# Kernel optimization log

Measured on AMD Instinct MI355X. Metric: run time of the kernel, lower is better.

Reference implementation:

```python
import jax, jax.numpy as jnp
import numpy as np

HIDDEN_DIM = 1024
NUM_HEADS = 16
HEAD_DIM = HIDDEN_DIM // NUM_HEADS
SCALAR_NORM = float(np.sqrt(HIDDEN_DIM / NUM_HEADS))


def setup_inputs() -> dict:
    key = jax.random.key(0)
    k1, k2 = jax.random.split(key)
    B, N, D = 2, 2048, HIDDEN_DIM
    x = jax.random.normal(k1, (B, N, D), dtype=jnp.float32)
    # torch Linear weight shape: (3D, D); xavier_uniform-like scale
    limit = float(np.sqrt(6.0 / (D + 3 * D)))
    W_qkv = jax.random.uniform(k2, (3 * D, D), dtype=jnp.float32, minval=-limit, maxval=limit)
    return {"x": x, "W_qkv": W_qkv}


def reference(x, W_qkv):
    b, n, d = x.shape
    h, hd = NUM_HEADS, HEAD_DIM
    qkv = x @ W_qkv.T  # (B, N, 3D)
    q, k, v = jnp.split(qkv, 3, axis=-1)
    # (B, H, N, hd)
    q = q.reshape(b, n, h, hd).transpose(0, 2, 1, 3)
    k = k.reshape(b, n, h, hd).transpose(0, 2, 1, 3)
    v = v.reshape(b, n, h, hd).transpose(0, 2, 1, 3)
    scores = jnp.einsum('bhik,bhjk->bhij', q, k) / SCALAR_NORM
    attn = jax.nn.softmax(scores, axis=-1)
    out = jnp.einsum('bhij,bhjk->bhik', attn, v)
    return out.transpose(0, 2, 1, 3).reshape(b, n, d)
```

## Files before the change

kernel.cpp:

```cpp
#include <hip/hip_runtime.h>
#include <hip/hip_bf16.h>

#define SEQ 2048
#define DMODEL 1024
#define NHEADS 16
#define HD 64
#define BATCH 2

typedef short bf16x8 __attribute__((ext_vector_type(8)));
typedef float f32x4 __attribute__((ext_vector_type(4)));

static __device__ inline ushort f2bf(float f) {
    unsigned u = __float_as_uint(f);
    return (ushort)((u + 0x7fffu + ((u >> 16) & 1u)) >> 16);
}

static __device__ inline unsigned pk2bf(float a, float b) {
    __hip_bfloat162 h = __float22bfloat162_rn(make_float2(a, b));
    union { __hip_bfloat162 h; unsigned u; } c; c.h = h;
    return c.u;
}

static __device__ inline void async16(const ushort* g, ushort* l) {
    __builtin_amdgcn_global_load_lds((const __attribute__((address_space(1))) void*)g,
                                     (__attribute__((address_space(3))) void*)l, 16, 0, 0);
}

__global__ void cvt2(const float* __restrict__ a, ushort* __restrict__ da, int na,
                     const float* __restrict__ b, ushort* __restrict__ db, int nb) {
    long i = (long)(blockIdx.x * blockDim.x + threadIdx.x) * 4;
    const float* s; ushort* d;
    if (i < na) { s = a + i; d = da + i; }
    else { long j = i - na; if (j >= nb) return; s = b + j; d = db + j; }
    float4 v = *(const float4*)s;
    ushort4 o; o.x = f2bf(v.x); o.y = f2bf(v.y); o.z = f2bf(v.z); o.w = f2bf(v.w);
    *(ushort4*)d = o;
}

union GemmSmem {
    struct { ushort A[128 * 64]; ushort B[128 * 64]; } st;
    ushort C[128 * 128];
};

__global__ __launch_bounds__(256) void qkv_gemm(
        const ushort* __restrict__ X, const ushort* __restrict__ W,
        ushort* __restrict__ Qd, ushort* __restrict__ Kd, ushort* __restrict__ Vd) {
    __shared__ GemmSmem sm;
    const int t = threadIdx.x;
    const int lane = t & 63, l15 = lane & 15, quad = lane >> 4;
    const int w = t >> 6, wm = w >> 1, wn = w & 1;
    const int gm = blockIdx.x, gn = blockIdx.y;
    const int srow = t >> 3, scol = (t & 7) * 8;

    f32x4 acc[4][4] = {};

    for (int kt = 0; kt < 16; ++kt) {
        const int k0 = kt * 64;
        __syncthreads();
#pragma unroll
        for (int inst = 0; inst < 4; ++inst) {
            async16(&X[(gm * 128 + inst * 32 + srow) * 1024 + k0 + scol], &sm.st.A[inst * 2048 + t * 8]);
            async16(&W[(gn * 128 + inst * 32 + srow) * 1024 + k0 + scol], &sm.st.B[inst * 2048 + t * 8]);
        }
        __syncthreads();
#pragma unroll
        for (int ks = 0; ks < 2; ++ks) {
            const int kk = ks * 32 + quad * 8;
            bf16x8 af[4], bfr[4];
#pragma unroll
            for (int i = 0; i < 4; ++i) {
                af[i]  = *(const bf16x8*)&sm.st.A[(wm * 64 + i * 16 + l15) * 64 + kk];
                bfr[i] = *(const bf16x8*)&sm.st.B[(wn * 64 + i * 16 + l15) * 64 + kk];
            }
#pragma unroll
            for (int i = 0; i < 4; ++i)
#pragma unroll
                for (int j = 0; j < 4; ++j)
                    acc[i][j] = __builtin_amdgcn_mfma_f32_16x16x32_bf16(af[i], bfr[j], acc[i][j], 0, 0, 0);
        }
    }

    __syncthreads();
    const float sc = (gn < 8) ? (0.125f * 1.44269504f) : 1.0f;
#pragma unroll
    for (int i = 0; i < 4; ++i)
#pragma unroll
        for (int reg = 0; reg < 4; ++reg) {
            const int row = wm * 64 + i * 16 + quad * 4 + reg;
            const int sw = (row & 7) * 8;
#pragma unroll
            for (int jp = 0; jp < 4; jp += 2) {
                unsigned u = pk2bf(acc[i][jp][reg] * sc, acc[i][jp + 1][reg] * sc);
                sm.C[row * 128 + ((wn * 64 + jp * 16 + l15) ^ sw)] = (ushort)u;
                sm.C[row * 128 + ((wn * 64 + (jp + 1) * 16 + l15) ^ sw)] = (ushort)(u >> 16);
            }
        }
    __syncthreads();

    const int which = gn >> 3;
    ushort* dst = (which == 0) ? Qd : ((which == 1) ? Kd : Vd);
    const int rloc = t >> 4, l = t & 15;
#pragma unroll
    for (int pass = 0; pass < 8; ++pass) {
        const int r = pass * 16 + rloc;
        bf16x8 v = *(const bf16x8*)&sm.C[r * 128 + ((l * 8) ^ ((r & 7) * 8))];
        const int ng = gm * 128 + r;
        const int b = ng >> 11, n = ng & 2047;
        const int cl = (gn * 128 + l * 8) & 1023;
        const int h = cl >> 6, hd = cl & 63;
        *(bf16x8*)&dst[(((b * NHEADS + h) * SEQ) + n) * HD + hd] = v;
    }
}

__global__ __launch_bounds__(256) void tr_v(const ushort* __restrict__ src, ushort* __restrict__ dst) {
    __shared__ ushort sT[64][72];
    const int t = threadIdx.x;
    const int bh = blockIdx.y, nt = blockIdx.x;
    const int r0 = t >> 3, c8 = (t & 7) * 8;
    const ushort* sp = src + ((long)bh * SEQ + nt * 64) * HD;
#pragma unroll
    for (int rr = 0; rr < 64; rr += 32)
        *(bf16x8*)&sT[rr + r0][c8] = *(const bf16x8*)&sp[(rr + r0) * HD + c8];
    __syncthreads();
    ushort* dp = dst + (long)bh * HD * SEQ + nt * 64;
#pragma unroll
    for (int rr = 0; rr < 64; rr += 32) {
        const int hd = rr + r0;
        bf16x8 v;
#pragma unroll
        for (int j = 0; j < 8; ++j) v[j] = (short)sT[c8 + j][hd];
        *(bf16x8*)&dp[(long)hd * SEQ + c8] = v;
    }
}

__global__ __launch_bounds__(128, 2) void attn_kernel(
        const ushort* __restrict__ Q, const ushort* __restrict__ K,
        const ushort* __restrict__ VT, float* __restrict__ O) {
    __shared__ ushort sK[64][72];
    __shared__ ushort sVT[64][72];
    __shared__ ushort sP[64][72];
    const int t = threadIdx.x;
    const int lane = t & 63, l15 = lane & 15, quad = lane >> 4;
    const int w = t >> 6;
    const int qt = blockIdx.x, bh = blockIdx.y;
    const ushort* Qp = Q + ((long)bh * SEQ + qt * 64) * HD;
    const ushort* Kp = K + (long)bh * SEQ * HD;
    const ushort* Vp = VT + (long)bh * HD * SEQ;
    const int r0 = t >> 3, c8 = (t & 7) * 8;

    bf16x8 aq[2][2];
#pragma unroll
    for (int st = 0; st < 2; ++st)
#pragma unroll
        for (int kc = 0; kc < 2; ++kc)
            aq[st][kc] = *(const bf16x8*)&Qp[(w * 32 + st * 16 + l15) * HD + kc * 32 + quad * 8];

    f32x4 accO[2][4] = {};
    f32x4 accL[2] = {};
    bf16x8 ones;
#pragma unroll
    for (int j = 0; j < 8; ++j) ones[j] = (short)0x3F80;

    for (int kt = 0; kt < 32; ++kt) {
        __syncthreads();
#pragma unroll
        for (int rr = 0; rr < 64; rr += 16) {
            *(bf16x8*)&sK[rr + r0][c8]  = *(const bf16x8*)&Kp[(kt * 64 + rr + r0) * HD + c8];
            *(bf16x8*)&sVT[rr + r0][c8] = *(const bf16x8*)&Vp[(rr + r0) * SEQ + kt * 64 + c8];
        }
        __syncthreads();

        f32x4 s[2][4];
#pragma unroll
        for (int st = 0; st < 2; ++st)
#pragma unroll
            for (int nb = 0; nb < 4; ++nb) {
                f32x4 z = {};
                z = __builtin_amdgcn_mfma_f32_16x16x32_bf16(aq[st][0], *(const bf16x8*)&sK[nb * 16 + l15][quad * 8], z, 0, 0, 0);
                z = __builtin_amdgcn_mfma_f32_16x16x32_bf16(aq[st][1], *(const bf16x8*)&sK[nb * 16 + l15][32 + quad * 8], z, 0, 0, 0);
                s[st][nb] = z;
            }

#pragma unroll
        for (int st = 0; st < 2; ++st)
#pragma unroll
            for (int r = 0; r < 4; ++r) {
                const int row = w * 32 + st * 16 + quad * 4 + r;
#pragma unroll
                for (int nb = 0; nb < 4; nb += 2) {
                    unsigned u = pk2bf(exp2f(s[st][nb][r]), exp2f(s[st][nb + 1][r]));
                    sP[row][(nb * 16 + l15) ^ (quad << 4)] = (ushort)u;
                    sP[row][((nb + 1) * 16 + l15) ^ (quad << 4)] = (ushort)(u >> 16);
                }
            }

        bf16x8 ap[2][2];
#pragma unroll
        for (int st = 0; st < 2; ++st)
#pragma unroll
            for (int kb = 0; kb < 2; ++kb)
                ap[st][kb] = *(const bf16x8*)&sP[w * 32 + st * 16 + l15][(kb * 32 + quad * 8) ^ ((l15 & 12) << 2)];

#pragma unroll
        for (int st = 0; st < 2; ++st) {
#pragma unroll
            for (int ob = 0; ob < 4; ++ob)
#pragma unroll
                for (int kb = 0; kb < 2; ++kb)
                    accO[st][ob] = __builtin_amdgcn_mfma_f32_16x16x32_bf16(
                        ap[st][kb], *(const bf16x8*)&sVT[ob * 16 + l15][kb * 32 + quad * 8], accO[st][ob], 0, 0, 0);
#pragma unroll
            for (int kb = 0; kb < 2; ++kb)
                accL[st] = __builtin_amdgcn_mfma_f32_16x16x32_bf16(ap[st][kb], ones, accL[st], 0, 0, 0);
        }
    }

    const int b = bh >> 4, h = bh & 15;
#pragma unroll
    for (int st = 0; st < 2; ++st)
#pragma unroll
        for (int r = 0; r < 4; ++r) {
            const float inv = 1.0f / accL[st][r];
            const int row = qt * 64 + w * 32 + st * 16 + quad * 4 + r;
#pragma unroll
            for (int ob = 0; ob < 4; ++ob)
                O[((long)b * SEQ + row) * DMODEL + h * HD + ob * 16 + l15] = accO[st][ob][r] * inv;
        }
}

extern "C" void kernel_launch(void* const* d_in, const int* in_sizes, int n_in,
                              void* d_out, int out_size, void* d_ws, size_t ws_size,
                              hipStream_t stream) {
    const float* x  = (const float*)d_in[0];
    const float* Wq = (const float*)d_in[1];
    float* out = (float*)d_out;

    const int NX = BATCH * SEQ * DMODEL;
    const int NW = 3 * DMODEL * DMODEL;
    const int NQKV = BATCH * NHEADS * SEQ * HD;

    ushort* xb = (ushort*)d_ws;
    ushort* wb = xb + NX;
    ushort* q  = wb + NW;
    ushort* k  = q + NQKV;
    ushort* vtmp = k + NQKV;
    ushort* vt = xb;

    cvt2<<<(NX + NW) / 4 / 256, 256, 0, stream>>>(x, xb, NX, Wq, wb, NW);

    dim3 g1(4096 / 128, 3072 / 128);
    qkv_gemm<<<g1, 256, 0, stream>>>(xb, wb, q, k, vtmp);

    dim3 gt(SEQ / 64, BATCH * NHEADS);
    tr_v<<<gt, 256, 0, stream>>>(vtmp, vt);

    dim3 g2(SEQ / 64, BATCH * NHEADS);
    attn_kernel<<<g2, 128, 0, stream>>>(q, k, vt, out);
}
```

Measured before the change: 195.1 us.

## Enlarge attention query tile to 128 rows and double-buffer K/V in LDS

Each attention block now covers 128 query rows, with 64 per wave, so every K/V tile loaded into shared memory is reused by twice as many queries, and the grid is halved. K and V^T tiles are double-buffered: the next tile is staged while the current one is consumed, which leaves one barrier per iteration instead of two. K and V fragments are also read into registers once per tile and reused across all query subtiles. In exchange, register pressure rises, launch bounds drop to one block, and there are half as many blocks, which lowers wave occupancy and latency hiding.

```diff
diff --git a/kernel.cpp b/kernel.cpp
--- a/kernel.cpp
+++ b/kernel.cpp
@@ -133,99 +133,127 @@
     }
 }
 
-__global__ __launch_bounds__(128, 2) void attn_kernel(
+__global__ __launch_bounds__(128, 1) void attn_kernel(
         const ushort* __restrict__ Q, const ushort* __restrict__ K,
         const ushort* __restrict__ VT, float* __restrict__ O) {
-    __shared__ ushort sK[64][72];
-    __shared__ ushort sVT[64][72];
-    __shared__ ushort sP[64][72];
+    __shared__ ushort sK[2][64][72];
+    __shared__ ushort sVT[2][64][72];
+    __shared__ ushort sP[128][72];
     const int t = threadIdx.x;
     const int lane = t & 63, l15 = lane & 15, quad = lane >> 4;
     const int w = t >> 6;
     const int qt = blockIdx.x, bh = blockIdx.y;
-    const ushort* Qp = Q + ((long)bh * SEQ + qt * 64) * HD;
+    const ushort* Qp = Q + ((long)bh * SEQ + qt * 128) * HD;
     const ushort* Kp = K + (long)bh * SEQ * HD;
     const ushort* Vp = VT + (long)bh * HD * SEQ;
     const int r0 = t >> 3, c8 = (t & 7) * 8;
 
-    bf16x8 aq[2][2];
-#pragma unroll
-    for (int st = 0; st < 2; ++st)
+    bf16x8 aq[4][2];
+#pragma unroll
+    for (int st = 0; st < 4; ++st)
 #pragma unroll
         for (int kc = 0; kc < 2; ++kc)
-            aq[st][kc] = *(const bf16x8*)&Qp[(w * 32 + st * 16 + l15) * HD + kc * 32 + quad * 8];
-
-    f32x4 accO[2][4] = {};
-    f32x4 accL[2] = {};
+            aq[st][kc] = *(const bf16x8*)&Qp[(w * 64 + st * 16 + l15) * HD + kc * 32 + quad * 8];
+
+    f32x4 accO[4][4] = {};
+    f32x4 accL[4] = {};
     bf16x8 ones;
 #pragma unroll
     for (int j = 0; j < 8; ++j) ones[j] = (short)0x3F80;
 
+    const int pswz = (quad & 2) << 3;
+    const int rswz = (l15 & 8) << 1;
+
+#define STAGE(kt, buf)                                                              \
+    {                                                                               \
+        _Pragma("unroll")                                                           \
+        for (int rr = 0; rr < 64; rr += 16) {                                       \
+            const int r = rr + r0;                                                  \
+            *(bf16x8*)&sK[buf][r][c8]  = *(const bf16x8*)&Kp[((kt) * 64 + r) * HD + c8]; \
+            *(bf16x8*)&sVT[buf][r][c8] = *(const bf16x8*)&Vp[r * SEQ + (kt) * 64 + c8];  \
+        }                                                                           \
+    }
+
+    STAGE(0, 0)
+    __syncthreads();
+
     for (int kt = 0; kt < 32; ++kt) {
-        __syncthreads();
-#pragma unroll
-        for (int rr = 0; rr < 64; rr += 16) {
-            *(bf16x8*)&sK[rr + r0][c8]  = *(const bf16x8*)&Kp[(kt * 64 + rr + r0) * HD + c8];
-            *(bf16x8*)&sVT[rr + r0][c8] = *(const bf16x8*)&Vp[(rr + r0) * SEQ + kt * 64 + c8];
-        }
-        __syncthreads();
-
-        f32x4 s[2][4];
-#pragma unroll
-        for (int st = 0; st < 2; ++st)
+        const int buf = kt & 1;
+        if (kt + 1 < 32) STAGE(kt + 1, buf ^ 1)
+
+        bf16x8 bk[4][2];
+#pragma unroll
+        for (int nb = 0; nb < 4; ++nb)
+#pragma unroll
+            for (int kc = 0; kc < 2; ++kc)
+                bk[nb][kc] = *(const bf16x8*)&sK[buf][nb * 16 + l15][kc * 32 + quad * 8];
+
+        f32x4 s[4][4];
+#pragma unroll
+        for (int st = 0; st < 4; ++st)
 #pragma unroll
             for (int nb = 0; nb < 4; ++nb) {
                 f32x4 z = {};
-                z = __builtin_amdgcn_mfma_f32_16x16x32_bf16(aq[st][0], *(const bf16x8*)&sK[nb * 16 + l15][quad * 8], z, 0, 0, 0);
-                z = __builtin_amdgcn_mfma_f32_16x16x32_bf16(aq[st][1], *(const bf16x8*)&sK[nb * 16 + l15][32 + quad * 8], z, 0, 0, 0);
+                z = __builtin_amdgcn_mfma_f32_16x16x32_bf16(aq[st][0], bk[nb][0], z, 0, 0, 0);
+                z = __builtin_amdgcn_mfma_f32_16x16x32_bf16(aq[st][1], bk[nb][1], z, 0, 0, 0);
                 s[st][nb] = z;
             }
 
 #pragma unroll
-        for (int st = 0; st < 2; ++st)
+        for (int st = 0; st < 4; ++st)
 #pragma unroll
             for (int r = 0; r < 4; ++r) {
-                const int row = w * 32 + st * 16 + quad * 4 + r;
+                const int row = w * 64 + st * 16 + quad * 4 + r;
 #pragma unroll
                 for (int nb = 0; nb < 4; nb += 2) {
                     unsigned u = pk2bf(exp2f(s[st][nb][r]), exp2f(s[st][nb + 1][r]));
-                    sP[row][(nb * 16 + l15) ^ (quad << 4)] = (ushort)u;
-                    sP[row][((nb + 1) * 16 + l15) ^ (quad << 4)] = (ushort)(u >> 16);
+                    sP[row][(nb * 16 + l15) ^ pswz] = (ushort)u;
+                    sP[row][((nb + 1) * 16 + l15) ^ pswz] = (ushort)(u >> 16);
                 }
             }
 
-        bf16x8 ap[2][2];
-#pragma unroll
-        for (int st = 0; st < 2; ++st)
+        bf16x8 ap[4][2];
+#pragma unroll
+        for (int st = 0; st < 4; ++st)
 #pragma unroll
             for (int kb = 0; kb < 2; ++kb)
-                ap[st][kb] = *(const bf16x8*)&sP[w * 32 + st * 16 + l15][(kb * 32 + quad * 8) ^ ((l15 & 12) << 2)];
-
-#pragma unroll
-        for (int st = 0; st < 2; ++st) {
+                ap[st][kb] = *(const bf16x8*)&sP[w * 64 + st * 16 + l15][(kb * 32 + quad * 8) ^ rswz];
+
+        bf16x8 bv[4][2];
+#pragma unroll
+        for (int ob = 0; ob < 4; ++ob)
+#pragma unroll
+            for (int kb = 0; kb < 2; ++kb)
+                bv[ob][kb] = *(const bf16x8*)&sVT[buf][ob * 16 + l15][kb * 32 + quad * 8];
+
+#pragma unroll
+        for (int st = 0; st < 4; ++st) {
 #pragma unroll
             for (int ob = 0; ob < 4; ++ob)
 #pragma unroll
                 for (int kb = 0; kb < 2; ++kb)
                     accO[st][ob] = __builtin_amdgcn_mfma_f32_16x16x32_bf16(
-                        ap[st][kb], *(const bf16x8*)&sVT[ob * 16 + l15][kb * 32 + quad * 8], accO[st][ob], 0, 0, 0);
+                        ap[st][kb], bv[ob][kb], accO[st][ob], 0, 0, 0);
 #pragma unroll
             for (int kb = 0; kb < 2; ++kb)
                 accL[st] = __builtin_amdgcn_mfma_f32_16x16x32_bf16(ap[st][kb], ones, accL[st], 0, 0, 0);
         }
+
+        __syncthreads();
     }
 
     const int b = bh >> 4, h = bh & 15;
 #pragma unroll
-    for (int st = 0; st < 2; ++st)
+    for (int st = 0; st < 4; ++st)
 #pragma unroll
         for (int r = 0; r < 4; ++r) {
             const float inv = 1.0f / accL[st][r];
-            const int row = qt * 64 + w * 32 + st * 16 + quad * 4 + r;
+            const int row = qt * 128 + w * 64 + st * 16 + quad * 4 + r;
 #pragma unroll
             for (int ob = 0; ob < 4; ++ob)
                 O[((long)b * SEQ + row) * DMODEL + h * HD + ob * 16 + l15] = accO[st][ob][r] * inv;
         }
+#undef STAGE
 }
 
 extern "C" void kernel_launch(void* const* d_in, const int* in_sizes, int n_in,
@@ -254,6 +282,6 @@
     dim3 gt(SEQ / 64, BATCH * NHEADS);
     tr_v<<<gt, 256, 0, stream>>>(vtmp, vt);
 
-    dim3 g2(SEQ / 64, BATCH * NHEADS);
+    dim3 g2(SEQ / 128, BATCH * NHEADS);
     attn_kernel<<<g2, 128, 0, stream>>>(q, k, vt, out);
 }
```

Measured after the change: 262.3 us. +34.5%, slower.

## Double-buffer K tiles in LDS and load V fragments directly from global

Applied to the files above, without the earlier changes.

K tiles are now double-buffered in shared memory. The next tile is prefetched into registers while the current one is being computed, and stored to the other buffer at the end of the iteration, which leaves one barrier per iteration instead of two. V^T MFMA operands are read straight from global memory into registers rather than staged through LDS, and K operands are hoisted into registers before the MFMAs. The sP swizzle pattern is also changed. The aim is to hide global load latency and cut LDS traffic and syncs, at the cost of more registers and uncoalesced direct V loads that are not shared across the two waves.

```diff
diff --git a/kernel.cpp b/kernel.cpp
--- a/kernel.cpp
+++ b/kernel.cpp
@@ -136,8 +136,7 @@
 __global__ __launch_bounds__(128, 2) void attn_kernel(
         const ushort* __restrict__ Q, const ushort* __restrict__ K,
         const ushort* __restrict__ VT, float* __restrict__ O) {
-    __shared__ ushort sK[64][72];
-    __shared__ ushort sVT[64][72];
+    __shared__ ushort sK[2][64][72];
     __shared__ ushort sP[64][72];
     const int t = threadIdx.x;
     const int lane = t & 63, l15 = lane & 15, quad = lane >> 4;
@@ -161,14 +160,37 @@
 #pragma unroll
     for (int j = 0; j < 8; ++j) ones[j] = (short)0x3F80;
 
+    const int pswz = (quad & 2) << 3;
+    const int rswz = (l15 & 8) << 1;
+
+#pragma unroll
+    for (int p = 0; p < 4; ++p)
+        *(bf16x8*)&sK[0][p * 16 + r0][c8] = *(const bf16x8*)&Kp[(p * 16 + r0) * HD + c8];
+    __syncthreads();
+
     for (int kt = 0; kt < 32; ++kt) {
-        __syncthreads();
-#pragma unroll
-        for (int rr = 0; rr < 64; rr += 16) {
-            *(bf16x8*)&sK[rr + r0][c8]  = *(const bf16x8*)&Kp[(kt * 64 + rr + r0) * HD + c8];
-            *(bf16x8*)&sVT[rr + r0][c8] = *(const bf16x8*)&Vp[(rr + r0) * SEQ + kt * 64 + c8];
-        }
-        __syncthreads();
+        const int buf = kt & 1;
+
+        bf16x8 kreg[4];
+        if (kt < 31) {
+#pragma unroll
+            for (int p = 0; p < 4; ++p)
+                kreg[p] = *(const bf16x8*)&Kp[((kt + 1) * 64 + p * 16 + r0) * HD + c8];
+        }
+
+        bf16x8 bv[4][2];
+#pragma unroll
+        for (int ob = 0; ob < 4; ++ob)
+#pragma unroll
+            for (int kb = 0; kb < 2; ++kb)
+                bv[ob][kb] = *(const bf16x8*)&Vp[(long)(ob * 16 + l15) * SEQ + kt * 64 + kb * 32 + quad * 8];
+
+        bf16x8 bk[4][2];
+#pragma unroll
+        for (int nb = 0; nb < 4; ++nb)
+#pragma unroll
+            for (int kc = 0; kc < 2; ++kc)
+                bk[nb][kc] = *(const bf16x8*)&sK[buf][nb * 16 + l15][kc * 32 + quad * 8];
 
         f32x4 s[2][4];
 #pragma unroll
@@ -176,8 +198,8 @@
 #pragma unroll
             for (int nb = 0; nb < 4; ++nb) {
                 f32x4 z = {};
-                z = __builtin_amdgcn_mfma_f32_16x16x32_bf16(aq[st][0], *(const bf16x8*)&sK[nb * 16 + l15][quad * 8], z, 0, 0, 0);
-                z = __builtin_amdgcn_mfma_f32_16x16x32_bf16(aq[st][1], *(const bf16x8*)&sK[nb * 16 + l15][32 + quad * 8], z, 0, 0, 0);
+                z = __builtin_amdgcn_mfma_f32_16x16x32_bf16(aq[st][0], bk[nb][0], z, 0, 0, 0);
+                z = __builtin_amdgcn_mfma_f32_16x16x32_bf16(aq[st][1], bk[nb][1], z, 0, 0, 0);
                 s[st][nb] = z;
             }
 
@@ -189,8 +211,8 @@
 #pragma unroll
                 for (int nb = 0; nb < 4; nb += 2) {
                     unsigned u = pk2bf(exp2f(s[st][nb][r]), exp2f(s[st][nb + 1][r]));
-                    sP[row][(nb * 16 + l15) ^ (quad << 4)] = (ushort)u;
-                    sP[row][((nb + 1) * 16 + l15) ^ (quad << 4)] = (ushort)(u >> 16);
+                    sP[row][(nb * 16 + l15) ^ pswz] = (ushort)u;
+                    sP[row][((nb + 1) * 16 + l15) ^ pswz] = (ushort)(u >> 16);
                 }
             }
 
@@ -199,7 +221,7 @@
         for (int st = 0; st < 2; ++st)
 #pragma unroll
             for (int kb = 0; kb < 2; ++kb)
-                ap[st][kb] = *(const bf16x8*)&sP[w * 32 + st * 16 + l15][(kb * 32 + quad * 8) ^ ((l15 & 12) << 2)];
+                ap[st][kb] = *(const bf16x8*)&sP[w * 32 + st * 16 + l15][(kb * 32 + quad * 8) ^ rswz];
 
 #pragma unroll
         for (int st = 0; st < 2; ++st) {
@@ -208,11 +230,18 @@
 #pragma unroll
                 for (int kb = 0; kb < 2; ++kb)
                     accO[st][ob] = __builtin_amdgcn_mfma_f32_16x16x32_bf16(
-                        ap[st][kb], *(const bf16x8*)&sVT[ob * 16 + l15][kb * 32 + quad * 8], accO[st][ob], 0, 0, 0);
+                        ap[st][kb], bv[ob][kb], accO[st][ob], 0, 0, 0);
 #pragma unroll
             for (int kb = 0; kb < 2; ++kb)
                 accL[st] = __builtin_amdgcn_mfma_f32_16x16x32_bf16(ap[st][kb], ones, accL[st], 0, 0, 0);
         }
+
+        if (kt < 31) {
+#pragma unroll
+            for (int p = 0; p < 4; ++p)
+                *(bf16x8*)&sK[buf ^ 1][p * 16 + r0][c8] = kreg[p];
+        }
+        __syncthreads();
     }
 
     const int b = bh >> 4, h = bh & 15;
```

After: 202.3 us. 3.7% more time.

## Drop shared memory in attention, compute S transposed to keep P in registers

Applied to the files above, without the earlier changes.

The attention kernel no longer stages K, V^T and P through LDS. It computes S^T = K·Q^T so that each lane's exp'd scores can be packed directly as the A operand of 16x16x16 bf16 MFMAs for the P·V product, which removes the sP round trip and all block barriers. The row sum is now accumulated in scalar registers and reduced with shuffles instead of a ones-vector MFMA. A 1D grid remaps block ids to interleave heads for L2 locality. In exchange, K and V are read directly from global memory by every wave with no sharing between the two waves in a block, and the PV product uses the smaller k16 MFMA shape, which issues twice as many instructions.

```diff
diff --git a/kernel.cpp b/kernel.cpp
--- a/kernel.cpp
+++ b/kernel.cpp
@@ -8,6 +8,7 @@
 #define BATCH 2
 
 typedef short bf16x8 __attribute__((ext_vector_type(8)));
+typedef short s16x4 __attribute__((ext_vector_type(4)));
 typedef float f32x4 __attribute__((ext_vector_type(4)));
 
 static __device__ inline ushort f2bf(float f) {
@@ -19,6 +20,15 @@
     __hip_bfloat162 h = __float22bfloat162_rn(make_float2(a, b));
     union { __hip_bfloat162 h; unsigned u; } c; c.h = h;
     return c.u;
+}
+
+static __device__ inline f32x4 mfma16(s16x4 a, s16x4 b, f32x4 c) {
+#if __has_builtin(__builtin_amdgcn_mfma_f32_16x16x16bf16_1k)
+    return __builtin_amdgcn_mfma_f32_16x16x16bf16_1k(a, b, c, 0, 0, 0);
+#else
+    asm("v_mfma_f32_16x16x16_bf16 %0, %1, %2, %0" : "+v"(c) : "v"(a), "v"(b));
+    return c;
+#endif
 }
 
 static __device__ inline void async16(const ushort* g, ushort* l) {
@@ -136,83 +146,75 @@
 __global__ __launch_bounds__(128, 2) void attn_kernel(
         const ushort* __restrict__ Q, const ushort* __restrict__ K,
         const ushort* __restrict__ VT, float* __restrict__ O) {
-    __shared__ ushort sK[64][72];
-    __shared__ ushort sVT[64][72];
-    __shared__ ushort sP[64][72];
     const int t = threadIdx.x;
     const int lane = t & 63, l15 = lane & 15, quad = lane >> 4;
     const int w = t >> 6;
-    const int qt = blockIdx.x, bh = blockIdx.y;
-    const ushort* Qp = Q + ((long)bh * SEQ + qt * 64) * HD;
+    const int id = blockIdx.x;
+    const int bh = (id & 7) * 4 + ((id >> 3) & 3);
+    const int qt = id >> 5;
+    const ushort* Qp = Q + ((long)bh * SEQ + qt * 64 + w * 32) * HD;
     const ushort* Kp = K + (long)bh * SEQ * HD;
     const ushort* Vp = VT + (long)bh * HD * SEQ;
-    const int r0 = t >> 3, c8 = (t & 7) * 8;
 
     bf16x8 aq[2][2];
 #pragma unroll
     for (int st = 0; st < 2; ++st)
 #pragma unroll
         for (int kc = 0; kc < 2; ++kc)
-            aq[st][kc] = *(const bf16x8*)&Qp[(w * 32 + st * 16 + l15) * HD + kc * 32 + quad * 8];
+            aq[st][kc] = *(const bf16x8*)&Qp[(st * 16 + l15) * HD + kc * 32 + quad * 8];
 
     f32x4 accO[2][4] = {};
-    f32x4 accL[2] = {};
-    bf16x8 ones;
-#pragma unroll
-    for (int j = 0; j < 8; ++j) ones[j] = (short)0x3F80;
+    float accL[2] = {0.f, 0.f};
 
     for (int kt = 0; kt < 32; ++kt) {
-        __syncthreads();
-#pragma unroll
-        for (int rr = 0; rr < 64; rr += 16) {
-            *(bf16x8*)&sK[rr + r0][c8]  = *(const bf16x8*)&Kp[(kt * 64 + rr + r0) * HD + c8];
-            *(bf16x8*)&sVT[rr + r0][c8] = *(const bf16x8*)&Vp[(rr + r0) * SEQ + kt * 64 + c8];
-        }
-        __syncthreads();
-
-        f32x4 s[2][4];
+        const int kv0 = kt * 64;
+
+        bf16x8 bk[4][2];
+#pragma unroll
+        for (int nb = 0; nb < 4; ++nb)
+#pragma unroll
+            for (int kc = 0; kc < 2; ++kc)
+                bk[nb][kc] = *(const bf16x8*)&Kp[(long)(kv0 + nb * 16 + l15) * HD + kc * 32 + quad * 8];
+
+        s16x4 bv[4][4];
+#pragma unroll
+        for (int ob = 0; ob < 4; ++ob)
+#pragma unroll
+            for (int nb = 0; nb < 4; ++nb)
+                bv[ob][nb] = *(const s16x4*)&Vp[(long)(ob * 16 + l15) * SEQ + kv0 + nb * 16 + quad * 4];
+
+        s16x4 pa[2][4];
 #pragma unroll
         for (int st = 0; st < 2; ++st)
 #pragma unroll
             for (int nb = 0; nb < 4; ++nb) {
                 f32x4 z = {};
-                z = __builtin_amdgcn_mfma_f32_16x16x32_bf16(aq[st][0], *(const bf16x8*)&sK[nb * 16 + l15][quad * 8], z, 0, 0, 0);
-                z = __builtin_amdgcn_mfma_f32_16x16x32_bf16(aq[st][1], *(const bf16x8*)&sK[nb * 16 + l15][32 + quad * 8], z, 0, 0, 0);
-                s[st][nb] = z;
+                z = __builtin_amdgcn_mfma_f32_16x16x32_bf16(bk[nb][0], aq[st][0], z, 0, 0, 0);
+                z = __builtin_amdgcn_mfma_f32_16x16x32_bf16(bk[nb][1], aq[st][1], z, 0, 0, 0);
+                const float e0 = __builtin_amdgcn_exp2f(z[0]);
+                const float e1 = __builtin_amdgcn_exp2f(z[1]);
+                const float e2 = __builtin_amdgcn_exp2f(z[2]);
+                const float e3 = __builtin_amdgcn_exp2f(z[3]);
+                accL[st] += (e0 + e1) + (e2 + e3);
+                union { unsigned u[2]; s16x4 v; } pk;
+                pk.u[0] = pk2bf(e0, e1);
+                pk.u[1] = pk2bf(e2, e3);
+                pa[st][nb] = pk.v;
             }
 
 #pragma unroll
         for (int st = 0; st < 2; ++st)
 #pragma unroll
-            for (int r = 0; r < 4; ++r) {
-                const int row = w * 32 + st * 16 + quad * 4 + r;
-#pragma unroll
-                for (int nb = 0; nb < 4; nb += 2) {
-                    unsigned u = pk2bf(exp2f(s[st][nb][r]), exp2f(s[st][nb + 1][r]));
-                    sP[row][(nb * 16 + l15) ^ (quad << 4)] = (ushort)u;
-                    sP[row][((nb + 1) * 16 + l15) ^ (quad << 4)] = (ushort)(u >> 16);
-                }
-            }
-
-        bf16x8 ap[2][2];
-#pragma unroll
-        for (int st = 0; st < 2; ++st)
-#pragma unroll
-            for (int kb = 0; kb < 2; ++kb)
-                ap[st][kb] = *(const bf16x8*)&sP[w * 32 + st * 16 + l15][(kb * 32 + quad * 8) ^ ((l15 & 12) << 2)];
-
-#pragma unroll
-        for (int st = 0; st < 2; ++st) {
-#pragma unroll
             for (int ob = 0; ob < 4; ++ob)
 #pragma unroll
-                for (int kb = 0; kb < 2; ++kb)
-                    accO[st][ob] = __builtin_amdgcn_mfma_f32_16x16x32_bf16(
-                        ap[st][kb], *(const bf16x8*)&sVT[ob * 16 + l15][kb * 32 + quad * 8], accO[st][ob], 0, 0, 0);
-#pragma unroll
-            for (int kb = 0; kb < 2; ++kb)
-                accL[st] = __builtin_amdgcn_mfma_f32_16x16x32_bf16(ap[st][kb], ones, accL[st], 0, 0, 0);
-        }
+                for (int nb = 0; nb < 4; ++nb)
+                    accO[st][ob] = mfma16(pa[st][nb], bv[ob][nb], accO[st][ob]);
+    }
+
+#pragma unroll
+    for (int st = 0; st < 2; ++st) {
+        accL[st] += __shfl_xor(accL[st], 16);
+        accL[st] += __shfl_xor(accL[st], 32);
     }
 
     const int b = bh >> 4, h = bh & 15;
@@ -220,7 +222,8 @@
     for (int st = 0; st < 2; ++st)
 #pragma unroll
         for (int r = 0; r < 4; ++r) {
-            const float inv = 1.0f / accL[st][r];
+            const float Lq = __shfl(accL[st], quad * 4 + r);
+            const float inv = 1.0f / Lq;
             const int row = qt * 64 + w * 32 + st * 16 + quad * 4 + r;
 #pragma unroll
             for (int ob = 0; ob < 4; ++ob)
@@ -254,6 +257,5 @@
     dim3 gt(SEQ / 64, BATCH * NHEADS);
     tr_v<<<gt, 256, 0, stream>>>(vtmp, vt);
 
-    dim3 g2(SEQ / 64, BATCH * NHEADS);
-    attn_kernel<<<g2, 128, 0, stream>>>(q, k, vt, out);
-}
+    attn_kernel<<<1024, 128, 0, stream>>>(q, k, vt, out);
+}
```

After: 290.0 us. +48.7%, slower.
